# Kernel tuning notes

Hardware: AMD Instinct MI355X
Metric: run time of the kernel (lower is better)

## Reference

```python
import jax, jax.numpy as jnp
import numpy as np

N_NODES = 50000
N_EDGES = 800000
EMBED = 128
HEADS = 8
HEAD_DIM = EMBED // HEADS  # 16
HIDDEN = 512
EPS = 1e-5
SLOPE = 0.2  # DGL GATConv default negative_slope


def setup_inputs() -> dict:
    key = jax.random.key(0)
    ks = jax.random.split(key, 16)
    s = 0.05
    return {
        "x": jax.random.normal(ks[0], (N_NODES, EMBED), dtype=jnp.float32),
        "src": jax.random.randint(ks[1], (N_EDGES,), 0, N_NODES),
        "dst": jax.random.randint(ks[2], (N_EDGES,), 0, N_NODES),
        # GATConv params: fc weight stored as [in, out] (i.e. torch weight transposed)
        "W": jax.random.normal(ks[3], (EMBED, HEADS * HEAD_DIM), dtype=jnp.float32) * s,
        "attn_l": jax.random.normal(ks[4], (HEADS, HEAD_DIM), dtype=jnp.float32) * s,
        "attn_r": jax.random.normal(ks[5], (HEADS, HEAD_DIM), dtype=jnp.float32) * s,
        "gat_bias": jnp.zeros((EMBED,), dtype=jnp.float32),
        # BatchNorm1d affine params (training-mode batch stats used in math)
        "gamma1": jnp.ones((EMBED,), dtype=jnp.float32),
        "beta1": jnp.zeros((EMBED,), dtype=jnp.float32),
        "gamma2": jnp.ones((EMBED,), dtype=jnp.float32),
        "beta2": jnp.zeros((EMBED,), dtype=jnp.float32),
        # FFN weights stored as [in, out]
        "W1": jax.random.normal(ks[6], (EMBED, HIDDEN), dtype=jnp.float32) * s,
        "b1": jnp.zeros((HIDDEN,), dtype=jnp.float32),
        "W2": jax.random.normal(ks[7], (HIDDEN, EMBED), dtype=jnp.float32) * s,
        "b2": jnp.zeros((EMBED,), dtype=jnp.float32),
    }


def _batchnorm(y, gamma, beta):
    mu = jnp.mean(y, axis=0)
    var = jnp.var(y, axis=0)  # biased variance, as torch BN uses for normalization
    return gamma * (y - mu) * jax.lax.rsqrt(var + EPS) + beta


def reference(x, src, dst, W, attn_l, attn_r, gat_bias,
              gamma1, beta1, gamma2, beta2, W1, b1, W2, b2):
    N = x.shape[0]
    # ---- GATConv ----
    feat = (x @ W).reshape(N, HEADS, HEAD_DIM)              # [N,H,D]
    el = jnp.sum(feat * attn_l, axis=-1)                    # [N,H]
    er = jnp.sum(feat * attn_r, axis=-1)                    # [N,H]
    e = jax.nn.leaky_relu(el[src] + er[dst], SLOPE)         # [E,H]
    # segment softmax over incoming edges of each dst node
    m = jax.ops.segment_max(e, dst, num_segments=N)         # [N,H] (-inf for empty)
    ex = jnp.exp(e - m[dst])                                # [E,H]
    denom = jax.ops.segment_sum(ex, dst, num_segments=N)    # [N,H]
    a = ex / denom[dst]                                     # [E,H]
    msg = feat[src] * a[:, :, None]                         # [E,H,D]
    rst = jax.ops.segment_sum(msg, dst, num_segments=N)     # [N,H,D]
    rst = rst + gat_bias.reshape(HEADS, HEAD_DIM)
    h = x + rst.reshape(N, EMBED)                           # skip connection
    # ---- FFN block: BN -> skip(MLP) -> BN ----
    h = _batchnorm(h, gamma1, beta1)
    y = jax.nn.relu(h @ W1 + b1) @ W2 + b2
    h = _batchnorm(h + y, gamma2, beta2)
    return h
```

## Files before the change

kernel.cpp:

```cpp
#include <hip/hip_runtime.h>

#define NCH 128
#define NH  8
#define HID 512
#define SLOPE 0.2f
#define BN_EPS 1e-5f
#define LDP 136
#define NPW 4

typedef __attribute__((ext_vector_type(8))) short short8;
typedef __attribute__((ext_vector_type(4))) float floatx4;

__device__ inline unsigned short f2bf(float f) {
  unsigned u = __float_as_uint(f);
  u += 0x7fffu + ((u >> 16) & 1u);
  return (unsigned short)(u >> 16);
}
__device__ inline float bflo(unsigned u) { return __uint_as_float(u << 16); }
__device__ inline float bfhi(unsigned u) { return __uint_as_float(u & 0xffff0000u); }

__global__ void prep_all(const float* __restrict__ W, unsigned short* __restrict__ WT,
                         const float* __restrict__ W1, unsigned short* __restrict__ w1f,
                         const float* __restrict__ W2, unsigned short* __restrict__ w2f,
                         float* __restrict__ stats, int* __restrict__ cnt, int N) {
  int b = blockIdx.x, tid = threadIdx.x;
  if (b < 64) {
    int i = b * 256 + tid;
    int n = i >> 7, k = i & 127;
    WT[i] = f2bf(W[k * NCH + n]);
  } else if (b < 320) {
    int i = (b - 64) * 256 + tid;
    int ntile = i >> 11, kk = (i >> 9) & 3, lane = (i >> 3) & 63, j = i & 7;
    int k = kk * 32 + (lane >> 4) * 8 + j;
    int n = ntile * 16 + (lane & 15);
    w1f[i] = f2bf(W1[k * HID + n]);
  } else if (b < 576) {
    int i = (b - 320) * 256 + tid;
    int ch = i >> 14, nt = (i >> 11) & 7, kk = (i >> 9) & 3, lane = (i >> 3) & 63, j = i & 7;
    int k = ch * 128 + kk * 32 + (lane >> 4) * 8 + j;
    int n = nt * 16 + (lane & 15);
    w2f[i] = f2bf(W2[k * NCH + n]);
  } else if (b < 596) {
    int i = (b - 576) * 256 + tid;
    ((float4*)stats)[i] = make_float4(0.f, 0.f, 0.f, 0.f);
  } else {
    int i = (b - 596) * 256 + tid;
    int n4 = (N + 3) >> 2;
    if (i < n4) ((int4*)cnt)[i] = make_int4(0, 0, 0, 0);
  }
}

__global__ __launch_bounds__(256) void feat_hist(const float* __restrict__ x,
                                                 const unsigned short* __restrict__ WT,
                                                 const float* __restrict__ attn_r,
                                                 unsigned short* __restrict__ featb,
                                                 float* __restrict__ er,
                                                 int N,
                                                 const int* __restrict__ dst, int* __restrict__ cnt,
                                                 int E, int FB) {
  __shared__ unsigned short rowX[64 * LDP];
  __shared__ unsigned short wt[128 * LDP];
  __shared__ float arL[128];
  if (blockIdx.x >= FB) {
    int i = (blockIdx.x - FB) * 256 + threadIdx.x;
    if (i < E) atomicAdd(&cnt[dst[i]], 1);
    return;
  }
  int tid = threadIdx.x;
  int r0 = blockIdx.x * 64;
  int lane = tid & 63, wid = tid >> 6;
  int quad = lane >> 4, lc = lane & 15;
  int mrow = (wid & 1) * 32;
  int chalf = (wid >> 1) * 64;

  if (tid < 128) arL[tid] = attn_r[tid];
  {
    int n = tid >> 1, kg = (tid & 1) * 64;
    const uint4* g = (const uint4*)(WT + n * NCH + kg);
    uint4* l = (uint4*)&wt[n * LDP + kg];
    for (int i = 0; i < 8; i++) l[i] = g[i];
  }
  {
    int r = tid >> 2, kg = (tid & 3) * 32;
    int gr = r0 + r;
    unsigned short tmp[32];
    if (gr < N) {
      const float4* gp = (const float4*)(x + (size_t)gr * NCH + kg);
      for (int i = 0; i < 8; i++) {
        float4 v = gp[i];
        tmp[i * 4 + 0] = f2bf(v.x); tmp[i * 4 + 1] = f2bf(v.y);
        tmp[i * 4 + 2] = f2bf(v.z); tmp[i * 4 + 3] = f2bf(v.w);
      }
    } else {
      for (int i = 0; i < 32; i++) tmp[i] = 0;
    }
    uint4* l = (uint4*)&rowX[r * LDP + kg];
    const uint4* s = (const uint4*)tmp;
    for (int i = 0; i < 4; i++) l[i] = s[i];
  }
  __syncthreads();

  floatx4 acc[2][4];
  for (int rt = 0; rt < 2; rt++) for (int tt = 0; tt < 4; tt++) acc[rt][tt] = (floatx4)(0.f);
  for (int kk = 0; kk < 4; kk++) {
    short8 a0 = *(const short8*)&rowX[(mrow + lc) * LDP + kk * 32 + quad * 8];
    short8 a1 = *(const short8*)&rowX[(mrow + 16 + lc) * LDP + kk * 32 + quad * 8];
    for (int tt = 0; tt < 4; tt++) {
      short8 b = *(const short8*)&wt[(chalf + tt * 16 + lc) * LDP + kk * 32 + quad * 8];
      acc[0][tt] = __builtin_amdgcn_mfma_f32_16x16x32_bf16(a0, b, acc[0][tt], 0, 0, 0);
      acc[1][tt] = __builtin_amdgcn_mfma_f32_16x16x32_bf16(a1, b, acc[1][tt], 0, 0, 0);
    }
  }
  __syncthreads();
  for (int rt = 0; rt < 2; rt++)
    for (int tt = 0; tt < 4; tt++)
      for (int r = 0; r < 4; r++)
        rowX[(mrow + rt * 16 + quad * 4 + r) * LDP + chalf + tt * 16 + lc] = f2bf(acc[rt][tt][r]);
  __syncthreads();
  {
    int r = tid >> 2, kg = (tid & 3) * 32;
    int gr = r0 + r;
    if (gr < N) {
      uint4* gp = (uint4*)(featb + (size_t)gr * NCH + kg);
      const uint4* l = (const uint4*)&rowX[r * LDP + kg];
      for (int i = 0; i < 4; i++) gp[i] = l[i];
    }
  }
  for (int p = tid; p < 512; p += 256) {
    int row = p >> 3, h = p & 7;
    int gr = r0 + row;
    if (gr < N) {
      const unsigned* rp = (const unsigned*)&rowX[row * LDP + h * 16];
      float sr = 0.f;
      for (int q = 0; q < 8; q++) {
        unsigned u = rp[q];
        int c = h * 16 + 2 * q;
        sr += bflo(u) * arL[c] + bfhi(u) * arL[c + 1];
      }
      er[gr * NH + h] = sr;
    }
  }
}

__global__ void scan_part(const int* __restrict__ cnt, int* __restrict__ off,
                          int* __restrict__ bsum, int N) {
  __shared__ int sh[256];
  int t = threadIdx.x, i = blockIdx.x * 256 + t;
  int v = (i < N) ? cnt[i] : 0;
  sh[t] = v; __syncthreads();
  for (int d = 1; d < 256; d <<= 1) {
    int u = (t >= d) ? sh[t - d] : 0;
    __syncthreads();
    sh[t] += u;
    __syncthreads();
  }
  if (i < N) off[i] = sh[t] - v;
  if (t == 255) bsum[blockIdx.x] = sh[255];
}

__global__ void scan_add2(int* __restrict__ off, const int* __restrict__ bsum,
                          int* __restrict__ cursor, int N, int nb) {
  __shared__ int sh[256];
  int t = threadIdx.x;
  int v = (t < nb) ? bsum[t] : 0;
  sh[t] = v; __syncthreads();
  for (int d = 1; d < 256; d <<= 1) {
    int u = (t >= d) ? sh[t - d] : 0;
    __syncthreads();
    sh[t] += u;
    __syncthreads();
  }
  int pref = (blockIdx.x > 0) ? sh[blockIdx.x - 1] : 0;
  int i = blockIdx.x * 256 + t;
  if (i < N) {
    int w = off[i] + pref;
    off[i] = w;
    cursor[i] = w;
  }
}

__global__ void edge_scatter(const int* __restrict__ src, const int* __restrict__ dst,
                             int* __restrict__ cursor, int* __restrict__ ssrc, int E) {
  int i = blockIdx.x * 256 + threadIdx.x;
  if (i < E) {
    int p = atomicAdd(&cursor[dst[i]], 1);
    ssrc[p] = src[i];
  }
}

__global__ __launch_bounds__(256) void gat_gather7(const int* __restrict__ ssrc,
                                                   const int* __restrict__ off,
                                                   const int* __restrict__ cnt,
                                                   const float* __restrict__ attn_l,
                                                   const float* __restrict__ er,
                                                   const unsigned short* __restrict__ featb,
                                                   const float* __restrict__ x,
                                                   const float* __restrict__ gatb,
                                                   float* __restrict__ hbuf,
                                                   float* __restrict__ stats, int N) {
  __shared__ float ps[4][128], pq[4][128];
  int tid = threadIdx.x;
  int lane = tid & 63, w = tid >> 6;
  int hme = lane >> 3;
  int c0 = 2 * lane;
  float2 al2 = *(const float2*)(attn_l + c0);
  float alx = al2.x, aly = al2.y;
  float gb0 = gatb[c0], gb1 = gatb[c0 + 1];
  float s0 = 0.f, s1 = 0.f, q0 = 0.f, q1 = 0.f;
  int base = blockIdx.x * (4 * NPW) + w * NPW;
  for (int j = 0; j < NPW; j++) {
    int node = base + j;
    if (node >= N) break;
    node = __builtin_amdgcn_readfirstlane(node);
    float erh = er[node * NH + hme];
    int beg = __builtin_amdgcn_readfirstlane(off[node]);
    int num = __builtin_amdgcn_readfirstlane(cnt[node]);
    const int* sp = ssrc + beg;
    float acc0 = 0.f, acc1 = 0.f, den = 0.f;
    int i = 0;
    for (; i + 8 <= num; i += 8) {
      int n0 = __builtin_amdgcn_readfirstlane(sp[i + 0]);
      int n1 = __builtin_amdgcn_readfirstlane(sp[i + 1]);
      int n2 = __builtin_amdgcn_readfirstlane(sp[i + 2]);
      int n3 = __builtin_amdgcn_readfirstlane(sp[i + 3]);
      int n4 = __builtin_amdgcn_readfirstlane(sp[i + 4]);
      int n5 = __builtin_amdgcn_readfirstlane(sp[i + 5]);
      int n6 = __builtin_amdgcn_readfirstlane(sp[i + 6]);
      int n7 = __builtin_amdgcn_readfirstlane(sp[i + 7]);
      unsigned f0 = ((const unsigned*)(featb + (size_t)n0 * NCH))[lane];
      unsigned f1 = ((const unsigned*)(featb + (size_t)n1 * NCH))[lane];
      unsigned f2 = ((const unsigned*)(featb + (size_t)n2 * NCH))[lane];
      unsigned f3 = ((const unsigned*)(featb + (size_t)n3 * NCH))[lane];
      unsigned f4 = ((const unsigned*)(featb + (size_t)n4 * NCH))[lane];
      unsigned f5 = ((const unsigned*)(featb + (size_t)n5 * NCH))[lane];
      unsigned f6 = ((const unsigned*)(featb + (size_t)n6 * NCH))[lane];
      unsigned f7 = ((const unsigned*)(featb + (size_t)n7 * NCH))[lane];
      float p0 = bflo(f0) * alx + bfhi(f0) * aly;
      float p1 = bflo(f1) * alx + bfhi(f1) * aly;
      float p2 = bflo(f2) * alx + bfhi(f2) * aly;
      float p3 = bflo(f3) * alx + bfhi(f3) * aly;
      float p4 = bflo(f4) * alx + bfhi(f4) * aly;
      float p5 = bflo(f5) * alx + bfhi(f5) * aly;
      float p6 = bflo(f6) * alx + bfhi(f6) * aly;
      float p7 = bflo(f7) * alx + bfhi(f7) * aly;
      p0 += __shfl_xor(p0, 1); p1 += __shfl_xor(p1, 1);
      p2 += __shfl_xor(p2, 1); p3 += __shfl_xor(p3, 1);
      p4 += __shfl_xor(p4, 1); p5 += __shfl_xor(p5, 1);
      p6 += __shfl_xor(p6, 1); p7 += __shfl_xor(p7, 1);
      p0 += __shfl_xor(p0, 2); p1 += __shfl_xor(p1, 2);
      p2 += __shfl_xor(p2, 2); p3 += __shfl_xor(p3, 2);
      p4 += __shfl_xor(p4, 2); p5 += __shfl_xor(p5, 2);
      p6 += __shfl_xor(p6, 2); p7 += __shfl_xor(p7, 2);
      p0 += __shfl_xor(p0, 4); p1 += __shfl_xor(p1, 4);
      p2 += __shfl_xor(p2, 4); p3 += __shfl_xor(p3, 4);
      p4 += __shfl_xor(p4, 4); p5 += __shfl_xor(p5, 4);
      p6 += __shfl_xor(p6, 4); p7 += __shfl_xor(p7, 4);
      float e0 = p0 + erh, e1 = p1 + erh, e2 = p2 + erh, e3 = p3 + erh;
      float e4 = p4 + erh, e5 = p5 + erh, e6 = p6 + erh, e7 = p7 + erh;
      e0 = e0 > 0.f ? e0 : SLOPE * e0;  e1 = e1 > 0.f ? e1 : SLOPE * e1;
      e2 = e2 > 0.f ? e2 : SLOPE * e2;  e3 = e3 > 0.f ? e3 : SLOPE * e3;
      e4 = e4 > 0.f ? e4 : SLOPE * e4;  e5 = e5 > 0.f ? e5 : SLOPE * e5;
      e6 = e6 > 0.f ? e6 : SLOPE * e6;  e7 = e7 > 0.f ? e7 : SLOPE * e7;
      float w0 = __expf(e0), w1 = __expf(e1), w2 = __expf(e2), w3 = __expf(e3);
      float w4 = __expf(e4), w5 = __expf(e5), w6 = __expf(e6), w7 = __expf(e7);
      acc0 += w0 * bflo(f0) + w1 * bflo(f1) + w2 * bflo(f2) + w3 * bflo(f3)
            + w4 * bflo(f4) + w5 * bflo(f5) + w6 * bflo(f6) + w7 * bflo(f7);
      acc1 += w0 * bfhi(f0) + w1 * bfhi(f1) + w2 * bfhi(f2) + w3 * bfhi(f3)
            + w4 * bfhi(f4) + w5 * bfhi(f5) + w6 * bfhi(f6) + w7 * bfhi(f7);
      den  += w0 + w1 + w2 + w3 + w4 + w5 + w6 + w7;
    }
    for (; i < num; i++) {
      int s = __builtin_amdgcn_readfirstlane(sp[i]);
      unsigned f = ((const unsigned*)(featb + (size_t)s * NCH))[lane];
      float p = bflo(f) * alx + bfhi(f) * aly;
      p += __shfl_xor(p, 1); p += __shfl_xor(p, 2); p += __shfl_xor(p, 4);
      float e = p + erh;
      e = e > 0.f ? e : SLOPE * e;
      float wv = __expf(e);
      acc0 += wv * bflo(f); acc1 += wv * bfhi(f); den += wv;
    }
    float inv = den > 0.f ? 1.f / den : 0.f;
    float2 xv = *(const float2*)(x + (size_t)node * NCH + c0);
    float h0 = xv.x + acc0 * inv + gb0;
    float h1 = xv.y + acc1 * inv + gb1;
    *(float2*)(hbuf + (size_t)node * NCH + c0) = make_float2(h0, h1);
    s0 += h0; s1 += h1; q0 += h0 * h0; q1 += h1 * h1;
  }
  ps[w][c0] = s0; ps[w][c0 + 1] = s1;
  pq[w][c0] = q0; pq[w][c0 + 1] = q1;
  __syncthreads();
  if (tid < 128) {
    float ss = ps[0][tid] + ps[1][tid] + ps[2][tid] + ps[3][tid];
    float qq = pq[0][tid] + pq[1][tid] + pq[2][tid] + pq[3][tid];
    int rep = blockIdx.x & 7;
    atomicAdd(&stats[rep * 128 + tid], ss);
    atomicAdd(&stats[1024 + rep * 128 + tid], qq);
  }
}

__global__ __launch_bounds__(512, 4) void ffn_mfma2(const float* __restrict__ hbuf,
                                                    const float* __restrict__ g1, const float* __restrict__ be1,
                                                    const unsigned short* __restrict__ w1f,
                                                    const unsigned short* __restrict__ w2f,
                                                    const float* __restrict__ b1, const float* __restrict__ b2,
                                                    float* __restrict__ t, float* __restrict__ stats, int N) {
  __shared__ unsigned short w1t[16384];
  __shared__ unsigned short w2t[16384];
  __shared__ unsigned short scr[8][512];
  __shared__ float b1L[512];
  __shared__ float psc[128], psh[128], b2L[128], csum[128], csq[128];
  int tid = threadIdx.x;
  int lane = tid & 63, wid = tid >> 6;
  int quad = lane >> 4, lc = lane & 15;
  int r0 = blockIdx.x * 128;

  b1L[tid] = b1[tid];
  if (tid < 128) {
    float s = 0.f, sq = 0.f;
    for (int r = 0; r < 8; r++) {
      s  += stats[r * 128 + tid];
      sq += stats[1024 + r * 128 + tid];
    }
    float m = s / (float)N;
    float v = sq / (float)N - m * m;
    float rsv = rsqrtf(v + BN_EPS);
    float scv = g1[tid] * rsv;
    psc[tid] = scv;
    psh[tid] = be1[tid] - scv * m;
    b2L[tid] = b2[tid];
    csum[tid] = 0.f; csq[tid] = 0.f;
  }

  int arow = r0 + wid * 16 + lc;
  float4 av[4][2];
  for (int kk = 0; kk < 4; kk++) {
    if (arow < N) {
      const float4* p = (const float4*)(hbuf + (size_t)arow * NCH + kk * 32 + quad * 8);
      av[kk][0] = p[0]; av[kk][1] = p[1];
    } else {
      av[kk][0] = make_float4(0.f, 0.f, 0.f, 0.f);
      av[kk][1] = make_float4(0.f, 0.f, 0.f, 0.f);
    }
  }
  __syncthreads();

  short8 rowA[4];
  for (int kk = 0; kk < 4; kk++) {
    int c = kk * 32 + quad * 8;
    float4 s0 = *(float4*)&psc[c], s1 = *(float4*)&psc[c + 4];
    float4 h0 = *(float4*)&psh[c], h1 = *(float4*)&psh[c + 4];
    short8 r;
    r[0] = (short)f2bf(av[kk][0].x * s0.x + h0.x);
    r[1] = (short)f2bf(av[kk][0].y * s0.y + h0.y);
    r[2] = (short)f2bf(av[kk][0].z * s0.z + h0.z);
    r[3] = (short)f2bf(av[kk][0].w * s0.w + h0.w);
    r[4] = (short)f2bf(av[kk][1].x * s1.x + h1.x);
    r[5] = (short)f2bf(av[kk][1].y * s1.y + h1.y);
    r[6] = (short)f2bf(av[kk][1].z * s1.z + h1.z);
    r[7] = (short)f2bf(av[kk][1].w * s1.w + h1.w);
    rowA[kk] = r;
  }

  floatx4 acc2[8];
  for (int nt = 0; nt < 8; nt++) acc2[nt] = (floatx4)(0.f);

  for (int ch = 0; ch < 4; ch++) {
    __syncthreads();
    {
      const uint4* g1p = (const uint4*)(w1f + ch * 16384);
      const uint4* g2p = (const uint4*)(w2f + ch * 16384);
      uint4* l1 = (uint4*)w1t;
      uint4* l2 = (uint4*)w2t;
      for (int r = 0; r < 4; r++) {
        l1[tid + r * 512] = g1p[tid + r * 512];
        l2[tid + r * 512] = g2p[tid + r * 512];
      }
    }
    __syncthreads();

    for (int kk = 0; kk < 4; kk++) {
      floatx4 d0 = (floatx4)(0.f), d1 = (floatx4)(0.f);
      int t0 = 2 * kk, t1 = 2 * kk + 1;
      for (int kp = 0; kp < 4; kp++) {
        short8 a0 = *(const short8*)&w1t[(t0 * 4 + kp) * 512 + lane * 8];
        short8 a1 = *(const short8*)&w1t[(t1 * 4 + kp) * 512 + lane * 8];
        d0 = __builtin_amdgcn_mfma_f32_16x16x32_bf16(a0, rowA[kp], d0, 0, 0, 0);
        d1 = __builtin_amdgcn_mfma_f32_16x16x32_bf16(a1, rowA[kp], d1, 0, 0, 0);
      }
      {
        int bi0 = ch * 128 + t0 * 16 + 4 * quad;
        float4 bv0 = *(float4*)&b1L[bi0];
        float4 bv1 = *(float4*)&b1L[bi0 + 16];
        float v0, v1, v2, v3;
        unsigned lo, hi;
        int sidx;
        v0 = fmaxf(d0[0] + bv0.x, 0.f); v1 = fmaxf(d0[1] + bv0.y, 0.f);
        v2 = fmaxf(d0[2] + bv0.z, 0.f); v3 = fmaxf(d0[3] + bv0.w, 0.f);
        lo = (unsigned)f2bf(v0) | ((unsigned)f2bf(v1) << 16);
        hi = (unsigned)f2bf(v2) | ((unsigned)f2bf(v3) << 16);
        sidx = ((quad >> 1) * 16 + lc) * 8 + 4 * (quad & 1);
        *(uint2*)&scr[wid][sidx] = make_uint2(lo, hi);
        v0 = fmaxf(d1[0] + bv1.x, 0.f); v1 = fmaxf(d1[1] + bv1.y, 0.f);
        v2 = fmaxf(d1[2] + bv1.z, 0.f); v3 = fmaxf(d1[3] + bv1.w, 0.f);
        lo = (unsigned)f2bf(v0) | ((unsigned)f2bf(v1) << 16);
        hi = (unsigned)f2bf(v2) | ((unsigned)f2bf(v3) << 16);
        sidx = ((2 + (quad >> 1)) * 16 + lc) * 8 + 4 * (quad & 1);
        *(uint2*)&scr[wid][sidx] = make_uint2(lo, hi);
      }
      short8 a2 = *(const short8*)&scr[wid][lane * 8];
      for (int nt = 0; nt < 8; nt++) {
        short8 bfr = *(const short8*)&w2t[(nt * 4 + kk) * 512 + lane * 8];
        acc2[nt] = __builtin_amdgcn_mfma_f32_16x16x32_bf16(a2, bfr, acc2[nt], 0, 0, 0);
      }
    }
  }

  __syncthreads();
  {
    unsigned short* stash = w1t;
    for (int kk = 0; kk < 4; kk++)
      *(short8*)&stash[wid * 2048 + lc * 128 + kk * 32 + quad * 8] = rowA[kk];
  }
  __syncthreads();

  for (int nt = 0; nt < 8; nt++) {
    int col = nt * 16 + lc;
    float b2v = b2L[col];
    float s = 0.f, q = 0.f;
    for (int reg = 0; reg < 4; reg++) {
      int grow = r0 + wid * 16 + quad * 4 + reg;
      if (grow < N) {
        float base = bflo((unsigned)w1t[wid * 2048 + (quad * 4 + reg) * 128 + col]);
        float tv = base + acc2[nt][reg] + b2v;
        t[(size_t)grow * NCH + col] = tv;
        s += tv; q += tv * tv;
      }
    }
    s += __shfl_xor(s, 16); s += __shfl_xor(s, 32);
    q += __shfl_xor(q, 16); q += __shfl_xor(q, 32);
    if (quad == 0) { atomicAdd(&csum[col], s); atomicAdd(&csq[col], q); }
  }
  __syncthreads();
  if (tid < 128) {
    atomicAdd(&stats[16384 + tid * 16], csum[tid]);
    atomicAdd(&stats[18432 + tid * 16], csq[tid]);
  }
}

__global__ __launch_bounds__(256) void bn2_apply2(const float* __restrict__ t,
                                                  const float* __restrict__ g, const float* __restrict__ b,
                                                  const float* __restrict__ stats,
                                                  float* __restrict__ out, int N) {
  __shared__ float scs[128], shs[128];
  int tid = threadIdx.x;
  if (tid < 128) {
    float s = stats[16384 + tid * 16], sq = stats[18432 + tid * 16];
    float m = s / (float)N;
    float v = sq / (float)N - m * m;
    float rsv = rsqrtf(v + BN_EPS);
    float gg = g[tid] * rsv;
    scs[tid] = gg;
    shs[tid] = b[tid] - gg * m;
  }
  __syncthreads();
  int i = blockIdx.x * 256 + tid;
  int tot4 = N * 32;
  if (i < tot4) {
    float4 v = ((const float4*)t)[i];
    int c = (i & 31) * 4;
    float4 o;
    o.x = v.x * scs[c + 0] + shs[c + 0];
    o.y = v.y * scs[c + 1] + shs[c + 1];
    o.z = v.z * scs[c + 2] + shs[c + 2];
    o.w = v.w * scs[c + 3] + shs[c + 3];
    ((float4*)out)[i] = o;
  }
}

extern "C" void kernel_launch(void* const* d_in, const int* in_sizes, int n_in,
                              void* d_out, int out_size, void* d_ws, size_t ws_size,
                              hipStream_t stream) {
  const float* x       = (const float*)d_in[0];
  const int*   src     = (const int*)d_in[1];
  const int*   dst     = (const int*)d_in[2];
  const float* W       = (const float*)d_in[3];
  const float* attn_l  = (const float*)d_in[4];
  const float* attn_r  = (const float*)d_in[5];
  const float* gatb    = (const float*)d_in[6];
  const float* gamma1  = (const float*)d_in[7];
  const float* beta1   = (const float*)d_in[8];
  const float* gamma2  = (const float*)d_in[9];
  const float* beta2   = (const float*)d_in[10];
  const float* W1      = (const float*)d_in[11];
  const float* b1      = (const float*)d_in[12];
  const float* W2      = (const float*)d_in[13];
  const float* b2      = (const float*)d_in[14];
  float* out = (float*)d_out;

  const int N = in_sizes[0] / NCH;
  const int E = in_sizes[1];
  const int nb = (N + 255) / 256;
  const int EB = (E + 255) / 256;
  const int FB = (N + 63) / 64;

  float* hbuf  = (float*)d_ws;
  float* t     = hbuf + (size_t)N * NCH;
  float* er    = t + (size_t)N * NCH;
  float* stats = er + (size_t)N * NH;
  unsigned short* featb = (unsigned short*)(stats + 20480);
  unsigned short* WT    = featb + (size_t)N * NCH;
  unsigned short* w1f   = WT + NCH * NCH;
  unsigned short* w2f   = w1f + HID * NCH;
  int* cnt    = (int*)(w2f + HID * NCH);
  int* off    = cnt + N;
  int* cursor = off + N;
  int* bsum   = cursor + N;
  int* ssrc   = bsum + 256;

  const int cb = (((N + 3) / 4) + 255) / 256;
  prep_all<<<596 + cb, 256, 0, stream>>>(W, WT, W1, w1f, W2, w2f, stats, cnt, N);

  feat_hist<<<FB + EB, 256, 0, stream>>>(x, WT, attn_r, featb, er, N, dst, cnt, E, FB);

  scan_part<<<nb, 256, 0, stream>>>(cnt, off, bsum, N);
  scan_add2<<<nb, 256, 0, stream>>>(off, bsum, cursor, N, nb);
  edge_scatter<<<EB, 256, 0, stream>>>(src, dst, cursor, ssrc, E);

  gat_gather7<<<(N + 4 * NPW - 1) / (4 * NPW), 256, 0, stream>>>(ssrc, off, cnt, attn_l, er,
                                                                 featb, x, gatb, hbuf, stats, N);

  ffn_mfma2<<<(N + 127) / 128, 512, 0, stream>>>(hbuf, gamma1, beta1,
                                                 w1f, w2f, b1, b2, t, stats, N);

  bn2_apply2<<<(N * 32 + 255) / 256, 256, 0, stream>>>(t, gamma2, beta2, stats, out, N);
}
```

Baseline: 296.9 us.

## Replace global-atomic edge scatter with two-pass bucketed CSR build

Swaps the per-edge global atomicAdd scatter for a two-pass binning scheme. The first pass groups edges by 256-node bucket using shared-memory atomics and one global atomic per bucket per chunk. The second pass places each bucket's edges into final CSR positions using shared-memory cursors. The aim is to cut contended global atomics and random scattered writes, at the cost of an extra kernel launch and an intermediate buffer of edge pairs that is written and read back.

```diff
diff --git a/kernel.cpp b/kernel.cpp
--- a/kernel.cpp
+++ b/kernel.cpp
@@ -7,6 +7,7 @@
 #define BN_EPS 1e-5f
 #define LDP 136
 #define NPW 4
+#define CHUNK 2048
 
 typedef __attribute__((ext_vector_type(8))) short short8;
 typedef __attribute__((ext_vector_type(4))) float floatx4;
@@ -159,7 +160,7 @@
 }
 
 __global__ void scan_add2(int* __restrict__ off, const int* __restrict__ bsum,
-                          int* __restrict__ cursor, int N, int nb) {
+                          int* __restrict__ bktcur, int N, int nb) {
   __shared__ int sh[256];
   int t = threadIdx.x;
   int v = (t < nb) ? bsum[t] : 0;
@@ -175,16 +176,57 @@
   if (i < N) {
     int w = off[i] + pref;
     off[i] = w;
-    cursor[i] = w;
-  }
-}
-
-__global__ void edge_scatter(const int* __restrict__ src, const int* __restrict__ dst,
-                             int* __restrict__ cursor, int* __restrict__ ssrc, int E) {
-  int i = blockIdx.x * 256 + threadIdx.x;
-  if (i < E) {
-    int p = atomicAdd(&cursor[dst[i]], 1);
-    ssrc[p] = src[i];
+    if (t == 0) bktcur[blockIdx.x] = w;
+  }
+}
+
+__global__ __launch_bounds__(256) void bin_scatter(const int* __restrict__ src,
+                                                   const int* __restrict__ dst,
+                                                   int* __restrict__ bktcur,
+                                                   uint2* __restrict__ ebuf, int E) {
+  __shared__ int bc[256];
+  __shared__ int bbase[256];
+  int tid = threadIdx.x;
+  int s = blockIdx.x * CHUNK;
+  int e = min(s + CHUNK, E);
+  bc[tid] = 0;
+  __syncthreads();
+  for (int i = s + tid; i < e; i += 256) atomicAdd(&bc[dst[i] >> 8], 1);
+  __syncthreads();
+  int c = bc[tid];
+  if (c > 0) bbase[tid] = atomicAdd(&bktcur[tid], c);
+  __syncthreads();
+  bc[tid] = 0;
+  __syncthreads();
+  for (int i = s + tid; i < e; i += 256) {
+    int d = dst[i];
+    int b = d >> 8;
+    int r = atomicAdd(&bc[b], 1);
+    ebuf[bbase[b] + r] = make_uint2((unsigned)src[i], (unsigned)d);
+  }
+}
+
+__global__ __launch_bounds__(256) void final_scatter(const uint2* __restrict__ ebuf,
+                                                     const int* __restrict__ off,
+                                                     int* __restrict__ ssrc,
+                                                     int E, int N, int NBK) {
+  __shared__ int lcur[256];
+  __shared__ int sbeg, send;
+  int tid = threadIdx.x;
+  int b = blockIdx.x;
+  int n0 = b * 256;
+  int node = n0 + tid;
+  lcur[tid] = (node < N) ? off[node] : 0;
+  if (tid == 0) {
+    sbeg = off[n0];
+    send = (b == NBK - 1) ? E : off[n0 + 256];
+  }
+  __syncthreads();
+  int beg = sbeg, end = send;
+  for (int i = beg + tid; i < end; i += 256) {
+    uint2 ed = ebuf[i];
+    int r = atomicAdd(&lcur[(int)ed.y - n0], 1);
+    ssrc[r] = (int)ed.x;
   }
 }
 
@@ -502,6 +544,7 @@
   const int nb = (N + 255) / 256;
   const int EB = (E + 255) / 256;
   const int FB = (N + 63) / 64;
+  const int BB = (E + CHUNK - 1) / CHUNK;
 
   float* hbuf  = (float*)d_ws;
   float* t     = hbuf + (size_t)N * NCH;
@@ -513,9 +556,10 @@
   unsigned short* w2f   = w1f + HID * NCH;
   int* cnt    = (int*)(w2f + HID * NCH);
   int* off    = cnt + N;
-  int* cursor = off + N;
-  int* bsum   = cursor + N;
+  int* bktcur = off + N;
+  int* bsum   = bktcur + 256;
   int* ssrc   = bsum + 256;
+  uint2* ebuf = (uint2*)(ssrc + E);
 
   const int cb = (((N + 3) / 4) + 255) / 256;
   prep_all<<<596 + cb, 256, 0, stream>>>(W, WT, W1, w1f, W2, w2f, stats, cnt, N);
@@ -523,8 +567,10 @@
   feat_hist<<<FB + EB, 256, 0, stream>>>(x, WT, attn_r, featb, er, N, dst, cnt, E, FB);
 
   scan_part<<<nb, 256, 0, stream>>>(cnt, off, bsum, N);
-  scan_add2<<<nb, 256, 0, stream>>>(off, bsum, cursor, N, nb);
-  edge_scatter<<<EB, 256, 0, stream>>>(src, dst, cursor, ssrc, E);
+  scan_add2<<<nb, 256, 0, stream>>>(off, bsum, bktcur, N, nb);
+
+  bin_scatter<<<BB, 256, 0, stream>>>(src, dst, bktcur, ebuf, E);
+  final_scatter<<<nb, 256, 0, stream>>>(ebuf, off, ssrc, E, N, nb);
 
   gat_gather7<<<(N + 4 * NPW - 1) / (4 * NPW), 256, 0, stream>>>(ssrc, off, cnt, attn_l, er,
                                                                  featb, x, gatb, hbuf, stats, N);
```

New measurement: 272.6 us. 8.2% less time.
